# Kernel optimization log

Measured on AMD Instinct MI355X. Metric: run time of the kernel, lower is better.

The kernel has to match this reference:

```python
import jax, jax.numpy as jnp
import numpy as np

NUM = 512
SIGMA = 0.2

def approx_heaviside(x):
    # ApproxHeaviside forward: hard step (0/1); sigma only affects the surrogate gradient.
    return (x > 0).astype(x.dtype)

def setup_inputs() -> dict:
    key = jax.random.key(0)
    k1, k2 = jax.random.split(key)
    inputs = jax.random.normal(k1, (8, 4096, NUM), dtype=jnp.float32)
    w = jax.random.normal(k2, (NUM, NUM), dtype=jnp.float32) * 0.02
    b = jnp.zeros((NUM,), dtype=jnp.float32)
    return {"inputs": inputs, "w": w, "b": b}

def reference(inputs, w, b):
    # zero the diagonal of w (fill_diagonal_(0))
    w1 = w * (1.0 - jnp.eye(NUM, dtype=w.dtype))
    # inhib = rinputs @ w1 + b over all tokens, vectorized
    inhib = jnp.einsum('bsn,nm->bsm', inputs, w1) + b
    gate = approx_heaviside(inhib)
    # diag_embed(inhib) then matmul == elementwise multiply by the gate
    return inputs * gate
```

## Files before the change

### kernel.cpp

```cpp
#include <hip/hip_runtime.h>
#include <stdint.h>


#define NUMD 512
#define EPS 1e-3f
#define FLCAP 512u
#define SA 4096.0f
#define SW 8192.0f
#define INV_S (1.0f / 33554432.0f)
#define TILE_F16 4096
#define SLAB_F16 (16 * TILE_F16)

typedef _Float16 f16;
typedef _Float16 f16x8 __attribute__((ext_vector_type(8)));
typedef float    f32x4 __attribute__((ext_vector_type(4)));

#define GLOAD_LDS16(g, l)                                                      \
  __builtin_amdgcn_global_load_lds(                                            \
      (const __attribute__((address_space(1))) void*)(g),                      \
      (__attribute__((address_space(3))) void*)(l), 16, 0, 0)

__global__ __launch_bounds__(256) void prep(
    const float* __restrict__ W, float* __restrict__ Wt,
    f16* __restrict__ WtH, f16* __restrict__ WtL)
{
    const int n = blockIdx.x;
    const int slab = n >> 7, rn = n & 127;
    const int srow = (rn >> 1) & 3;
    for (int k = threadIdx.x; k < NUMD; k += 256) {
        float v = W[(size_t)k * NUMD + n];
        if (k == n) v = 0.0f;
        Wt[(size_t)n * NUMD + k] = v;
        const float vs = v * SW;
        f16 h  = (f16)vs;
        f16 lo = (f16)(vs - (float)h);
        const int kt = k >> 5, kk = k & 31, c = kk >> 3, e = kk & 7;
        const int p = c ^ srow;
        const size_t off = (size_t)slab * SLAB_F16 + (size_t)kt * TILE_F16
                         + rn * 32 + p * 8 + e;
        WtH[off] = h; WtL[off] = lo;
    }
}

__global__ __launch_bounds__(256, 2) void li_mfma(
    const float* __restrict__ A,
    const f16* __restrict__ WtH, const f16* __restrict__ WtL,
    const float* __restrict__ Wt,
    const float* __restrict__ bias,
    float* __restrict__ out,
    int M, int cpx)
{
    __shared__ __align__(16) f16 lds[2][4][128][32];
    __shared__ unsigned flist[FLCAP];
    __shared__ unsigned lcnt;

    const int tid = threadIdx.x;
    const int l   = tid & 63;
    const int wv  = tid >> 6;
    const int wr  = wv >> 1;
    const int wc  = wv & 1;
    const int lG  = l >> 4;
    const int lM  = l & 15;

    int w = blockIdx.x;
    if (cpx) { const int xcd = w & 7, c = w >> 3; w = xcd * cpx + c; }
    const int m0  = (w >> 2) * 128;
    const int n0b = (w & 3) * 128;

    const size_t bOff = ((size_t)(n0b >> 7) * SLAB_F16) * 2 + wv * 2048 + l * 16;
    const char* pBH = (const char*)WtH;
    const char* pBL = (const char*)WtL;

#define STAGE_B(nb, ktb) do {                                                  \
    GLOAD_LDS16(pBH + bOff + (ktb),        &lds[nb][2][wv * 32][0]);           \
    GLOAD_LDS16(pBH + bOff + (ktb) + 1024, &lds[nb][2][wv * 32 + 16][0]);      \
    GLOAD_LDS16(pBL + bOff + (ktb),        &lds[nb][3][wv * 32][0]);           \
    GLOAD_LDS16(pBL + bOff + (ktb) + 1024, &lds[nb][3][wv * 32 + 16][0]);      \
  } while (0)

    const int r0 = tid >> 2, ca = tid & 3;
    const int r1 = r0 + 64;
    const float* aBase0 = A + (size_t)(m0 + r0) * NUMD + ca * 8;
    const float* aBase1 = A + (size_t)(m0 + r1) * NUMD + ca * 8;
    const int wo0 = r0 * 64 + ((ca ^ ((r0 >> 1) & 3)) << 4);
    const int wo1 = r1 * 64 + ((ca ^ ((r1 >> 1) & 3)) << 4);

    float4 av00, av01, av10, av11;

#define ALOAD(kt) do {                                                         \
    const float* s0 = aBase0 + (size_t)(kt) * 32;                              \
    const float* s1 = aBase1 + (size_t)(kt) * 32;                              \
    av00 = *(const float4*)s0; av01 = *(const float4*)(s0 + 4);                \
    av10 = *(const float4*)s1; av11 = *(const float4*)(s1 + 4);                \
  } while (0)

#define ACONV(nb) do {                                                         \
    const float a0[8] = {av00.x, av00.y, av00.z, av00.w,                       \
                         av01.x, av01.y, av01.z, av01.w};                      \
    const float a1[8] = {av10.x, av10.y, av10.z, av10.w,                       \
                         av11.x, av11.y, av11.z, av11.w};                      \
    f16x8 h0, lo0, h1, lo1;                                                    \
    _Pragma("unroll")                                                          \
    for (int e = 0; e < 8; ++e) {                                              \
        float as0 = a0[e] * SA; f16 hv0 = (f16)as0;                            \
        h0[e] = hv0; lo0[e] = (f16)(as0 - (float)hv0);                         \
        float as1 = a1[e] * SA; f16 hv1 = (f16)as1;                            \
        h1[e] = hv1; lo1[e] = (f16)(as1 - (float)hv1);                         \
    }                                                                          \
    *(f16x8*)((char*)&lds[nb][0][0][0] + wo0) = h0;                            \
    *(f16x8*)((char*)&lds[nb][1][0][0] + wo0) = lo0;                           \
    *(f16x8*)((char*)&lds[nb][0][0][0] + wo1) = h1;                            \
    *(f16x8*)((char*)&lds[nb][1][0][0] + wo1) = lo1;                           \
  } while (0)

    int aRd[4], bRd[4];
#pragma unroll
    for (int f = 0; f < 4; ++f) {
        const int mr = wr * 64 + f * 16 + lM;
        aRd[f] = mr * 64 + ((lG ^ ((mr >> 1) & 3)) << 4);
        const int nr = wc * 64 + f * 16 + lM;
        bRd[f] = nr * 64 + ((lG ^ ((nr >> 1) & 3)) << 4);
    }

    f32x4 acc[4][4];
#pragma unroll
    for (int i = 0; i < 4; ++i)
#pragma unroll
        for (int j = 0; j < 4; ++j) acc[i][j] = f32x4{0.f, 0.f, 0.f, 0.f};

    ALOAD(0);
    STAGE_B(0, 0);
    ACONV(0);

    const int NT = NUMD / 32;
    for (int kt = 0; kt < NT; ++kt) {
        const int cur = kt & 1;
        __syncthreads();

        if (kt + 1 < NT) {
            STAGE_B(cur ^ 1, (size_t)(kt + 1) * 8192);
            ALOAD(kt + 1);
        }

        const char* PAH = (const char*)&lds[cur][0][0][0];
        const char* PAL = (const char*)&lds[cur][1][0][0];
        const char* PBH = (const char*)&lds[cur][2][0][0];
        const char* PBL = (const char*)&lds[cur][3][0][0];

        f16x8 bh[4], bl[4];
#pragma unroll
        for (int fj = 0; fj < 4; ++fj) {
            bh[fj] = *(const f16x8*)(PBH + bRd[fj]);
            bl[fj] = *(const f16x8*)(PBL + bRd[fj]);
        }
        __builtin_amdgcn_s_setprio(1);
#pragma unroll
        for (int fi = 0; fi < 4; ++fi) {
            const f16x8 ah = *(const f16x8*)(PAH + aRd[fi]);
            const f16x8 al = *(const f16x8*)(PAL + aRd[fi]);
#pragma unroll
            for (int fj = 0; fj < 4; ++fj) {
                acc[fi][fj] = __builtin_amdgcn_mfma_f32_16x16x32_f16(ah, bh[fj], acc[fi][fj], 0, 0, 0);
                acc[fi][fj] = __builtin_amdgcn_mfma_f32_16x16x32_f16(ah, bl[fj], acc[fi][fj], 0, 0, 0);
                acc[fi][fj] = __builtin_amdgcn_mfma_f32_16x16x32_f16(al, bh[fj], acc[fi][fj], 0, 0, 0);
            }
        }
        __builtin_amdgcn_s_setprio(0);

        if (kt + 1 < NT) ACONV(cur ^ 1);
    }

    __syncthreads();
    float* cbuf = (float*)&lds[0][0][0][0];
    if (tid == 0) lcnt = 0;

#pragma unroll
    for (int fj = 0; fj < 4; ++fj) {
        const int cl = wc * 64 + fj * 16 + lM;
#pragma unroll
        for (int fi = 0; fi < 4; ++fi) {
            const int rl = wr * 64 + fi * 16 + lG * 4;
#pragma unroll
            for (int r = 0; r < 4; ++r)
                cbuf[(rl + r) * 128 + cl] = acc[fi][fj][r] * INV_S;
        }
    }
    __syncthreads();

    const int rcol = (tid & 31) * 4;
    const float4 bv4 = *(const float4*)(bias + n0b + rcol);
#pragma unroll
    for (int ch = 0; ch < 16; ++ch) {
        const int rrow = ch * 8 + (tid >> 5);
        const float4 v = *(const float4*)&cbuf[rrow * 128 + rcol];
        const size_t gi = (size_t)(m0 + rrow) * NUMD + n0b + rcol;
        const float4 x = *(const float4*)(A + gi);
        const float inh0 = v.x + bv4.x, inh1 = v.y + bv4.y;
        const float inh2 = v.z + bv4.z, inh3 = v.w + bv4.w;
        float4 o;
        o.x = (inh0 > 0.0f) ? x.x : 0.0f;
        o.y = (inh1 > 0.0f) ? x.y : 0.0f;
        o.z = (inh2 > 0.0f) ? x.z : 0.0f;
        o.w = (inh3 > 0.0f) ? x.w : 0.0f;
        *(float4*)(out + gi) = o;
        if (__builtin_fabsf(inh0) <= EPS) { unsigned p = atomicAdd(&lcnt, 1u); if (p < FLCAP) flist[p] = (unsigned)(gi + 0); }
        if (__builtin_fabsf(inh1) <= EPS) { unsigned p = atomicAdd(&lcnt, 1u); if (p < FLCAP) flist[p] = (unsigned)(gi + 1); }
        if (__builtin_fabsf(inh2) <= EPS) { unsigned p = atomicAdd(&lcnt, 1u); if (p < FLCAP) flist[p] = (unsigned)(gi + 2); }
        if (__builtin_fabsf(inh3) <= EPS) { unsigned p = atomicAdd(&lcnt, 1u); if (p < FLCAP) flist[p] = (unsigned)(gi + 3); }
    }

    __syncthreads();
    unsigned nf = lcnt; if (nf > FLCAP) nf = FLCAP;
    for (unsigned e = tid; e < nf; e += 256) {
        const unsigned code = flist[e];
        const int n = (int)(code & 511);
        const float* ar  = A  + (size_t)(code >> 9) * NUMD;
        const float* wr_ = Wt + (size_t)n * NUMD;
        float s = 0.0f;
#pragma unroll 8
        for (int k = 0; k < NUMD; ++k)
            s = fmaf(ar[k], wr_[k], s);
        const float inh = s + bias[n];
        out[code] = (inh > 0.0f) ? A[code] : 0.0f;
    }
#undef STAGE_B
#undef ALOAD
#undef ACONV
}

#define BM 128
#define BN 256
#define BK 16
#define TM 8
#define TN 16
#define NTF (NUMD / BK)

__global__ __launch_bounds__(256) void zero_diag_kernel(
    const float* __restrict__ W, float* __restrict__ Wz)
{
    const int f = (int)(blockIdx.x * blockDim.x + threadIdx.x) * 4;
    const int row = f >> 9, col0 = f & 511;
    float4 v = *(const float4*)(W + f);
    if (row == col0 + 0) v.x = 0.0f;
    if (row == col0 + 1) v.y = 0.0f;
    if (row == col0 + 2) v.z = 0.0f;
    if (row == col0 + 3) v.w = 0.0f;
    *(float4*)(Wz + f) = v;
}

template<bool ZDIAG>
__global__ __launch_bounds__(256, 1) void li_gemm_fp32(
    const float* __restrict__ A, const float* __restrict__ Wm,
    const float* __restrict__ bias, float* __restrict__ out, int M)
{
    __shared__ __align__(16) float As[2][BM][BK];
    __shared__ __align__(16) float Bs[2][BK][BN];
    const int tid = threadIdx.x, lane = tid & 63, wv = tid >> 6;
    const int tc = tid & 15, tr = tid >> 4;
    const int m0 = blockIdx.x * BM, n0 = blockIdx.y * BN;
    const int am0 = wv * 32 + (lane >> 2), am1 = am0 + 16;
    const int q0 = ((lane & 3) ^ ((am0 >> 3) & 3)) << 2;
    const int q1 = ((lane & 3) ^ ((am1 >> 3) & 3)) << 2;
    const float* aSrc0 = A + (size_t)(m0 + am0) * NUMD + q0;
    const float* aSrc1 = A + (size_t)(m0 + am1) * NUMD + q1;
    const float* wSrc = Wm + (size_t)(wv * 4) * NUMD + n0 + lane * 4;
    float acc[TM][TN];
#pragma unroll
    for (int i = 0; i < TM; ++i)
#pragma unroll
        for (int j = 0; j < TN; ++j) acc[i][j] = 0.0f;
    GLOAD_LDS16(aSrc0, &As[0][wv * 32][0]);
    GLOAD_LDS16(aSrc1, &As[0][wv * 32 + 16][0]);
#pragma unroll
    for (int r = 0; r < 4; ++r)
        GLOAD_LDS16(wSrc + (size_t)r * NUMD, &Bs[0][wv * 4 + r][0]);
    aSrc0 += BK; aSrc1 += BK; wSrc += (size_t)BK * NUMD;
    for (int kt = 0; kt < NTF; ++kt) {
        const int cur = kt & 1;
        __syncthreads();
        if (kt + 1 < NTF) {
            const int nb = cur ^ 1;
            GLOAD_LDS16(aSrc0, &As[nb][wv * 32][0]);
            GLOAD_LDS16(aSrc1, &As[nb][wv * 32 + 16][0]);
#pragma unroll
            for (int r = 0; r < 4; ++r)
                GLOAD_LDS16(wSrc + (size_t)r * NUMD, &Bs[nb][wv * 4 + r][0]);
            aSrc0 += BK; aSrc1 += BK; wSrc += (size_t)BK * NUMD;
        }
        if (ZDIAG) {
            const int kk = kt * BK;
            if (tid < BK) {
                const int col = kk + tid - n0;
                if (col >= 0 && col < BN) Bs[cur][tid][col] = 0.0f;
            }
            __syncthreads();
        }
#pragma unroll
        for (int g = 0; g < 4; ++g) {
            float4 af[TM];
#pragma unroll
            for (int i = 0; i < TM; ++i) {
                const int m = tr * TM + i;
                af[i] = *(const float4*)&As[cur][m][(g ^ ((m >> 3) & 3)) << 2];
            }
#pragma unroll
            for (int dk = 0; dk < 4; ++dk) {
                float b[TN];
#pragma unroll
                for (int c = 0; c < 4; ++c) {
                    float4 b4 = *(const float4*)&Bs[cur][g * 4 + dk][tc * 4 + 64 * c];
                    b[4*c+0] = b4.x; b[4*c+1] = b4.y; b[4*c+2] = b4.z; b[4*c+3] = b4.w;
                }
#pragma unroll
                for (int i = 0; i < TM; ++i) {
                    const float a = ((const float*)&af[i])[dk];
#pragma unroll
                    for (int j = 0; j < TN; ++j) acc[i][j] = fmaf(a, b[j], acc[i][j]);
                }
            }
        }
    }
    float bv[TN];
#pragma unroll
    for (int c = 0; c < 4; ++c) {
        float4 b4 = *(const float4*)(bias + n0 + tc * 4 + 64 * c);
        bv[4*c+0] = b4.x; bv[4*c+1] = b4.y; bv[4*c+2] = b4.z; bv[4*c+3] = b4.w;
    }
#pragma unroll
    for (int i = 0; i < TM; ++i) {
        const int gm = m0 + tr * TM + i;
        const float* inrow = A + (size_t)gm * NUMD + n0 + tc * 4;
        float* orow = out + (size_t)gm * NUMD + n0 + tc * 4;
#pragma unroll
        for (int c = 0; c < 4; ++c) {
            float4 x = *(const float4*)(inrow + 64 * c);
            float4 o;
            o.x = (acc[i][4*c+0] + bv[4*c+0] > 0.0f) ? x.x : 0.0f;
            o.y = (acc[i][4*c+1] + bv[4*c+1] > 0.0f) ? x.y : 0.0f;
            o.z = (acc[i][4*c+2] + bv[4*c+2] > 0.0f) ? x.z : 0.0f;
            o.w = (acc[i][4*c+3] + bv[4*c+3] > 0.0f) ? x.w : 0.0f;
            *(float4*)(orow + 64 * c) = o;
        }
    }
}

extern "C" void kernel_launch(void* const* d_in, const int* in_sizes, int n_in,
                              void* d_out, int out_size, void* d_ws, size_t ws_size,
                              hipStream_t stream) {
    const float* A    = (const float*)d_in[0];
    const float* W    = (const float*)d_in[1];
    const float* bias = (const float*)d_in[2];
    float* out        = (float*)d_out;
    const int M = in_sizes[0] / NUMD;

    const size_t need = (2u << 20) + 4096;

    if (ws_size >= need) {
        char* wsb = (char*)d_ws;
        float* Wt  = (float*)wsb;
        f16*   WtH = (f16*)(wsb + (1u << 20));
        f16*   WtL = (f16*)(wsb + (1u << 20) + (512u << 10));

        prep<<<dim3(NUMD), 256, 0, stream>>>(W, Wt, WtH, WtL);
        const int nwg = (M / 128) * (NUMD / 128);
        const int cpx = (nwg % 8 == 0) ? (nwg / 8) : 0;
        li_mfma<<<dim3(nwg), 256, 0, stream>>>(A, WtH, WtL, Wt, bias, out,
                                               M, cpx);
    } else {
        dim3 grid(M / BM, NUMD / BN);
        const size_t wbytes = (size_t)NUMD * NUMD * sizeof(float);
        if (ws_size >= wbytes) {
            float* Wz = (float*)d_ws;
            zero_diag_kernel<<<dim3(NUMD * NUMD / (4 * 256)), 256, 0, stream>>>(W, Wz);
            li_gemm_fp32<false><<<grid, 256, 0, stream>>>(A, Wz, bias, out, M);
        } else {
            li_gemm_fp32<true><<<grid, 256, 0, stream>>>(A, W, bias, out, M);
        }
    }
}
```

Before: 203.6 us.

## Drop A low-part split MFMA and write epilogue directly from accumulators

The activations are now split into a single f16 value instead of a hi/lo pair, which removes one of the three MFMAs per fragment, one LDS plane and its conversion and stores. The epilogue no longer stages results through LDS; each lane writes its gate output straight from the accumulators with scalar loads and stores. The launch-bounds occupancy hint is dropped. This lowers matmul work and LDS traffic but reduces precision of the inhibition sum, which leans on the near-zero fp32 fix-up list. The direct epilogue also replaces coalesced float4 accesses with strided scalar ones.

```diff
diff --git a/kernel.cpp b/kernel.cpp
--- a/kernel.cpp
+++ b/kernel.cpp
@@ -42,7 +42,7 @@
     }
 }
 
-__global__ __launch_bounds__(256, 2) void li_mfma(
+__global__ __launch_bounds__(256) void li_mfma(
     const float* __restrict__ A,
     const f16* __restrict__ WtH, const f16* __restrict__ WtL,
     const float* __restrict__ Wt,
@@ -50,7 +50,7 @@
     float* __restrict__ out,
     int M, int cpx)
 {
-    __shared__ __align__(16) f16 lds[2][4][128][32];
+    __shared__ __align__(16) f16 lds[2][3][128][32];
     __shared__ unsigned flist[FLCAP];
     __shared__ unsigned lcnt;
 
@@ -72,10 +72,10 @@
     const char* pBL = (const char*)WtL;
 
 #define STAGE_B(nb, ktb) do {                                                  \
-    GLOAD_LDS16(pBH + bOff + (ktb),        &lds[nb][2][wv * 32][0]);           \
-    GLOAD_LDS16(pBH + bOff + (ktb) + 1024, &lds[nb][2][wv * 32 + 16][0]);      \
-    GLOAD_LDS16(pBL + bOff + (ktb),        &lds[nb][3][wv * 32][0]);           \
-    GLOAD_LDS16(pBL + bOff + (ktb) + 1024, &lds[nb][3][wv * 32 + 16][0]);      \
+    GLOAD_LDS16(pBH + bOff + (ktb),        &lds[nb][1][wv * 32][0]);           \
+    GLOAD_LDS16(pBH + bOff + (ktb) + 1024, &lds[nb][1][wv * 32 + 16][0]);      \
+    GLOAD_LDS16(pBL + bOff + (ktb),        &lds[nb][2][wv * 32][0]);           \
+    GLOAD_LDS16(pBL + bOff + (ktb) + 1024, &lds[nb][2][wv * 32 + 16][0]);      \
   } while (0)
 
     const int r0 = tid >> 2, ca = tid & 3;
@@ -99,18 +99,14 @@
                          av01.x, av01.y, av01.z, av01.w};                      \
     const float a1[8] = {av10.x, av10.y, av10.z, av10.w,                       \
                          av11.x, av11.y, av11.z, av11.w};                      \
-    f16x8 h0, lo0, h1, lo1;                                                    \
+    f16x8 h0, h1;                                                              \
     _Pragma("unroll")                                                          \
     for (int e = 0; e < 8; ++e) {                                              \
-        float as0 = a0[e] * SA; f16 hv0 = (f16)as0;                            \
-        h0[e] = hv0; lo0[e] = (f16)(as0 - (float)hv0);                         \
-        float as1 = a1[e] * SA; f16 hv1 = (f16)as1;                            \
-        h1[e] = hv1; lo1[e] = (f16)(as1 - (float)hv1);                         \
+        h0[e] = (f16)(a0[e] * SA);                                             \
+        h1[e] = (f16)(a1[e] * SA);                                             \
     }                                                                          \
     *(f16x8*)((char*)&lds[nb][0][0][0] + wo0) = h0;                            \
-    *(f16x8*)((char*)&lds[nb][1][0][0] + wo0) = lo0;                           \
     *(f16x8*)((char*)&lds[nb][0][0][0] + wo1) = h1;                            \
-    *(f16x8*)((char*)&lds[nb][1][0][0] + wo1) = lo1;                           \
   } while (0)
 
     int aRd[4], bRd[4];
@@ -143,9 +139,8 @@
         }
 
         const char* PAH = (const char*)&lds[cur][0][0][0];
-        const char* PAL = (const char*)&lds[cur][1][0][0];
-        const char* PBH = (const char*)&lds[cur][2][0][0];
-        const char* PBL = (const char*)&lds[cur][3][0][0];
+        const char* PBH = (const char*)&lds[cur][1][0][0];
+        const char* PBL = (const char*)&lds[cur][2][0][0];
 
         f16x8 bh[4], bl[4];
 #pragma unroll
@@ -157,12 +152,10 @@
 #pragma unroll
         for (int fi = 0; fi < 4; ++fi) {
             const f16x8 ah = *(const f16x8*)(PAH + aRd[fi]);
-            const f16x8 al = *(const f16x8*)(PAL + aRd[fi]);
 #pragma unroll
             for (int fj = 0; fj < 4; ++fj) {
                 acc[fi][fj] = __builtin_amdgcn_mfma_f32_16x16x32_f16(ah, bh[fj], acc[fi][fj], 0, 0, 0);
                 acc[fi][fj] = __builtin_amdgcn_mfma_f32_16x16x32_f16(ah, bl[fj], acc[fi][fj], 0, 0, 0);
-                acc[fi][fj] = __builtin_amdgcn_mfma_f32_16x16x32_f16(al, bh[fj], acc[fi][fj], 0, 0, 0);
             }
         }
         __builtin_amdgcn_s_setprio(0);
@@ -171,42 +164,28 @@
     }
 
     __syncthreads();
-    float* cbuf = (float*)&lds[0][0][0][0];
     if (tid == 0) lcnt = 0;
+    __syncthreads();
 
 #pragma unroll
     for (int fj = 0; fj < 4; ++fj) {
-        const int cl = wc * 64 + fj * 16 + lM;
+        const int n = n0b + wc * 64 + fj * 16 + lM;
+        const float bvj = bias[n];
 #pragma unroll
         for (int fi = 0; fi < 4; ++fi) {
-            const int rl = wr * 64 + fi * 16 + lG * 4;
-#pragma unroll
-            for (int r = 0; r < 4; ++r)
-                cbuf[(rl + r) * 128 + cl] = acc[fi][fj][r] * INV_S;
-        }
-    }
-    __syncthreads();
-
-    const int rcol = (tid & 31) * 4;
-    const float4 bv4 = *(const float4*)(bias + n0b + rcol);
-#pragma unroll
-    for (int ch = 0; ch < 16; ++ch) {
-        const int rrow = ch * 8 + (tid >> 5);
-        const float4 v = *(const float4*)&cbuf[rrow * 128 + rcol];
-        const size_t gi = (size_t)(m0 + rrow) * NUMD + n0b + rcol;
-        const float4 x = *(const float4*)(A + gi);
-        const float inh0 = v.x + bv4.x, inh1 = v.y + bv4.y;
-        const float inh2 = v.z + bv4.z, inh3 = v.w + bv4.w;
-        float4 o;
-        o.x = (inh0 > 0.0f) ? x.x : 0.0f;
-        o.y = (inh1 > 0.0f) ? x.y : 0.0f;
-        o.z = (inh2 > 0.0f) ? x.z : 0.0f;
-        o.w = (inh3 > 0.0f) ? x.w : 0.0f;
-        *(float4*)(out + gi) = o;
-        if (__builtin_fabsf(inh0) <= EPS) { unsigned p = atomicAdd(&lcnt, 1u); if (p < FLCAP) flist[p] = (unsigned)(gi + 0); }
-        if (__builtin_fabsf(inh1) <= EPS) { unsigned p = atomicAdd(&lcnt, 1u); if (p < FLCAP) flist[p] = (unsigned)(gi + 1); }
-        if (__builtin_fabsf(inh2) <= EPS) { unsigned p = atomicAdd(&lcnt, 1u); if (p < FLCAP) flist[p] = (unsigned)(gi + 2); }
-        if (__builtin_fabsf(inh3) <= EPS) { unsigned p = atomicAdd(&lcnt, 1u); if (p < FLCAP) flist[p] = (unsigned)(gi + 3); }
+            const int mb = m0 + wr * 64 + fi * 16 + lG * 4;
+#pragma unroll
+            for (int r = 0; r < 4; ++r) {
+                const size_t idx = (size_t)(mb + r) * NUMD + n;
+                const float inh = acc[fi][fj][r] * INV_S + bvj;
+                const float x = A[idx];
+                out[idx] = (inh > 0.0f) ? x : 0.0f;
+                if (__builtin_fabsf(inh) <= EPS) {
+                    unsigned p = atomicAdd(&lcnt, 1u);
+                    if (p < FLCAP) flist[p] = (unsigned)idx;
+                }
+            }
+        }
     }
 
     __syncthreads();
```

New measurement: 224.1 us. 10.1% more time.
